# Kernel tuning notes

Measured on AMD Instinct MI355X. Metric: run time of the kernel, lower is better.

The kernel has to match this reference:

```python
import jax, jax.numpy as jnp
import numpy as np

K = 2  # number of propagation hops (SGConv K)
NEG_SLOPE = 0.1


def setup_inputs() -> dict:
    key = jax.random.key(0)
    k1, k2, k3, k4 = jax.random.split(key, 4)
    N, E, C_in, C_out = 50000, 800000, 128, 512
    x = jax.random.normal(k1, (N, C_in), dtype=jnp.float32)
    edge_index = jax.random.randint(k2, (2, E), 0, N, dtype=jnp.int64)
    W = jax.random.normal(k3, (C_out, C_in), dtype=jnp.float32) * (1.0 / np.sqrt(C_in))
    b = jax.random.normal(k4, (C_out,), dtype=jnp.float32) * 0.01
    return {"x": x, "edge_index": edge_index, "W": W, "b": b}


def reference(x, edge_index, W, b):
    N = x.shape[0]
    # gcn_norm with self-loops (PyG SGConv default: add_self_loops=True)
    loop = jnp.arange(N, dtype=edge_index.dtype)
    src = jnp.concatenate([edge_index[0], loop])  # message sources j
    dst = jnp.concatenate([edge_index[1], loop])  # aggregation targets i
    deg = jax.ops.segment_sum(jnp.ones_like(dst, dtype=x.dtype), dst, num_segments=N)
    dinv = jnp.where(deg > 0, jax.lax.rsqrt(deg), 0.0)
    norm = dinv[src] * dinv[dst]  # [E+N]
    h = x
    for _ in range(K):
        h = jax.ops.segment_sum(norm[:, None] * h[src], dst, num_segments=N)
    y = h @ W.T + b
    return jnp.where(y >= 0, y, NEG_SLOPE * y)  # LeakyReLU(0.1)
```

## Files before the change

### kernel.cpp

```cpp
#include <hip/hip_runtime.h>
#include <hip/hip_bf16.h>

#define CIN 128
#define COUT 512
#define NEG_SLOPE 0.1f

typedef __bf16 bf16x8 __attribute__((ext_vector_type(8)));
typedef float f32x4 __attribute__((ext_vector_type(4)));

static __device__ __forceinline__ unsigned short f2bf(float f) {
  unsigned int u = __builtin_bit_cast(unsigned int, f);
  unsigned int lsb = (u >> 16) & 1u;
  u += 0x7fffu + lsb;
  return (unsigned short)(u >> 16);
}
static __device__ __forceinline__ float bf_lo(unsigned int u) {
  return __builtin_bit_cast(float, u << 16);
}
static __device__ __forceinline__ float bf_hi(unsigned int u) {
  return __builtin_bit_cast(float, u & 0xffff0000u);
}
static __device__ __forceinline__ unsigned int pack2(float lo, float hi) {
  return (unsigned int)f2bf(lo) | ((unsigned int)f2bf(hi) << 16);
}

__global__ void detect_kernel(const int* __restrict__ raw, int* __restrict__ flag, int E) {
  __shared__ int any_nonzero;
  int tid = threadIdx.x;
  if (tid == 0) any_nonzero = 0;
  __syncthreads();
  int v1 = raw[2 * tid + 1];
  int v2 = raw[2 * (E / 2) + 2 * tid + 1];
  if (v1 != 0 || v2 != 0) atomicOr(&any_nonzero, 1);
  __syncthreads();
  if (tid == 0) *flag = any_nonzero ? 0 : 1;
}

__global__ void decode_count_kernel(const int* __restrict__ raw, const int* __restrict__ flag,
                                    int* __restrict__ srcA, int* __restrict__ dstA,
                                    int* __restrict__ rank, int* __restrict__ cnt,
                                    int E, int N) {
  int e = blockIdx.x * blockDim.x + threadIdx.x;
  if (e >= E) return;
  int is64 = *flag;
  int s, d;
  if (is64) {
    int2 sv = ((const int2*)raw)[e];
    int2 dv = ((const int2*)raw)[E + e];
    s = sv.x;
    d = dv.x;
  } else {
    s = raw[e];
    d = raw[E + e];
  }
  if ((unsigned)s >= (unsigned)N) s = 0;
  if ((unsigned)d >= (unsigned)N) d = 0;
  srcA[e] = s;
  dstA[e] = d;
  rank[e] = atomicAdd(&cnt[d], 1);
}

__global__ __launch_bounds__(256) void xscale_kernel(const float* __restrict__ x,
                                                     const int* __restrict__ cnt,
                                                     unsigned short* __restrict__ xs, int N) {
  int idx = blockIdx.x * blockDim.x + threadIdx.x;
  if (idx >= N * (CIN / 4)) return;
  int row = idx >> 5;
  float d = 1.0f / sqrtf((float)(cnt[row] + 1));
  float4 v = ((const float4*)x)[idx];
  ushort4 o;
  o.x = f2bf(v.x * d); o.y = f2bf(v.y * d); o.z = f2bf(v.z * d); o.w = f2bf(v.w * d);
  ((ushort4*)xs)[idx] = o;
}

__global__ __launch_bounds__(256) void scan1_kernel(const int* __restrict__ cnt,
                                                    int* __restrict__ rowptr,
                                                    int* __restrict__ bsum, int N) {
  __shared__ int buf[256];
  int tid = threadIdx.x;
  int base = blockIdx.x * 1024 + tid * 4;
  int v[4];
  int tot = 0;
#pragma unroll
  for (int k = 0; k < 4; ++k) {
    int i = base + k;
    v[k] = (i < N) ? cnt[i] : 0;
    tot += v[k];
  }
  buf[tid] = tot;
  __syncthreads();
  for (int off = 1; off < 256; off <<= 1) {
    int t = (tid >= off) ? buf[tid - off] : 0;
    __syncthreads();
    buf[tid] += t;
    __syncthreads();
  }
  int run = buf[tid] - tot;
  if (tid == 255) bsum[blockIdx.x] = buf[255];
#pragma unroll
  for (int k = 0; k < 4; ++k) {
    int i = base + k;
    if (i < N) rowptr[i] = run;
    run += v[k];
  }
}

__global__ void scan2_kernel(int* __restrict__ bsum, int nb) {
  __shared__ int buf[256];
  int tid = threadIdx.x;
  int v = (tid < nb) ? bsum[tid] : 0;
  buf[tid] = v;
  __syncthreads();
  for (int off = 1; off < 256; off <<= 1) {
    int t = (tid >= off) ? buf[tid - off] : 0;
    __syncthreads();
    buf[tid] += t;
    __syncthreads();
  }
  if (tid < nb) bsum[tid] = buf[tid] - v;
}

__global__ __launch_bounds__(256) void scan3_kernel(int* __restrict__ rowptr,
                                                    const int* __restrict__ bsum, int N) {
  int base = blockIdx.x * 1024 + threadIdx.x * 4;
  int off = bsum[blockIdx.x];
#pragma unroll
  for (int k = 0; k < 4; ++k) {
    int i = base + k;
    if (i < N) rowptr[i] += off;
  }
}

__global__ void scatter_kernel(const int* __restrict__ srcA, const int* __restrict__ dstA,
                               const int* __restrict__ rank, const int* __restrict__ rowptr,
                               int* __restrict__ col, int E) {
  int e = blockIdx.x * blockDim.x + threadIdx.x;
  if (e < E) col[rowptr[dstA[e]] + rank[e]] = srcA[e];
}

template <bool SQ>
__global__ __launch_bounds__(256) void hop_kernel(
    const unsigned short* __restrict__ Xs,
    const int* __restrict__ rowptr, const int* __restrict__ cnt,
    const int* __restrict__ col, unsigned short* __restrict__ Y, int N) {
  int lane = threadIdx.x & 63;
  int wid = threadIdx.x >> 6;
  int node = blockIdx.x * 4 + wid;
  if (node >= N) return;
  int sub = lane & 15;
  int grp = lane >> 4;
  int beg = rowptr[node];
  int num = cnt[node];
  const uint4* X4 = (const uint4*)Xs;
  float acc[8] = {0.f, 0.f, 0.f, 0.f, 0.f, 0.f, 0.f, 0.f};
  if (grp == 0) {
    uint4 s = X4[(size_t)node * 16 + sub];
    acc[0] = bf_lo(s.x); acc[1] = bf_hi(s.x);
    acc[2] = bf_lo(s.y); acc[3] = bf_hi(s.y);
    acc[4] = bf_lo(s.z); acc[5] = bf_hi(s.z);
    acc[6] = bf_lo(s.w); acc[7] = bf_hi(s.w);
  }
  const int* cp = col + beg;
  int kb = 0;
  for (; kb + 16 <= num; kb += 16) {
    int j0 = cp[kb + grp];
    int j1 = cp[kb + 4 + grp];
    int j2 = cp[kb + 8 + grp];
    int j3 = cp[kb + 12 + grp];
    uint4 v0 = X4[(size_t)j0 * 16 + sub];
    uint4 v1 = X4[(size_t)j1 * 16 + sub];
    uint4 v2 = X4[(size_t)j2 * 16 + sub];
    uint4 v3 = X4[(size_t)j3 * 16 + sub];
    acc[0] += bf_lo(v0.x); acc[1] += bf_hi(v0.x);
    acc[2] += bf_lo(v0.y); acc[3] += bf_hi(v0.y);
    acc[4] += bf_lo(v0.z); acc[5] += bf_hi(v0.z);
    acc[6] += bf_lo(v0.w); acc[7] += bf_hi(v0.w);
    acc[0] += bf_lo(v1.x); acc[1] += bf_hi(v1.x);
    acc[2] += bf_lo(v1.y); acc[3] += bf_hi(v1.y);
    acc[4] += bf_lo(v1.z); acc[5] += bf_hi(v1.z);
    acc[6] += bf_lo(v1.w); acc[7] += bf_hi(v1.w);
    acc[0] += bf_lo(v2.x); acc[1] += bf_hi(v2.x);
    acc[2] += bf_lo(v2.y); acc[3] += bf_hi(v2.y);
    acc[4] += bf_lo(v2.z); acc[5] += bf_hi(v2.z);
    acc[6] += bf_lo(v2.w); acc[7] += bf_hi(v2.w);
    acc[0] += bf_lo(v3.x); acc[1] += bf_hi(v3.x);
    acc[2] += bf_lo(v3.y); acc[3] += bf_hi(v3.y);
    acc[4] += bf_lo(v3.z); acc[5] += bf_hi(v3.z);
    acc[6] += bf_lo(v3.w); acc[7] += bf_hi(v3.w);
  }
  for (; kb < num; kb += 4) {
    int k = kb + grp;
    if (k < num) {
      int j0 = cp[k];
      uint4 v0 = X4[(size_t)j0 * 16 + sub];
      acc[0] += bf_lo(v0.x); acc[1] += bf_hi(v0.x);
      acc[2] += bf_lo(v0.y); acc[3] += bf_hi(v0.y);
      acc[4] += bf_lo(v0.z); acc[5] += bf_hi(v0.z);
      acc[6] += bf_lo(v0.w); acc[7] += bf_hi(v0.w);
    }
  }
#pragma unroll
  for (int r = 0; r < 8; ++r) acc[r] += __shfl_xor(acc[r], 16, 64);
#pragma unroll
  for (int r = 0; r < 8; ++r) acc[r] += __shfl_xor(acc[r], 32, 64);
  if (grp == 0) {
    float di = 1.0f / sqrtf((float)(num + 1));
    float sc = SQ ? di * di : di;
    uint4 o;
    o.x = pack2(acc[0] * sc, acc[1] * sc);
    o.y = pack2(acc[2] * sc, acc[3] * sc);
    o.z = pack2(acc[4] * sc, acc[5] * sc);
    o.w = pack2(acc[6] * sc, acc[7] * sc);
    ((uint4*)Y)[(size_t)node * 16 + sub] = o;
  }
}

__global__ void wconv_kernel(const float* __restrict__ W, unsigned short* __restrict__ Wbf, int n) {
  int i = blockIdx.x * blockDim.x + threadIdx.x;
  if (i < n) Wbf[i] = f2bf(W[i]);
}

__global__ __launch_bounds__(256) void gemm_kernel(
    const unsigned short* __restrict__ Abf, const unsigned short* __restrict__ Wbf,
    const float* __restrict__ bias, float* __restrict__ out, int M) {
  int wave = threadIdx.x >> 6;
  int lane = threadIdx.x & 63;
  int quad = lane >> 4;
  int l16 = lane & 15;
  int mbase = blockIdx.x * 32;

  int m0 = mbase + l16;
  int m1 = mbase + 16 + l16;
  bool v0 = m0 < M;
  bool v1 = m1 < M;

  bf16x8 af[2][4];
#pragma unroll
  for (int kk = 0; kk < 4; ++kk) {
    af[0][kk] = v0 ? *(const bf16x8*)(Abf + (size_t)m0 * CIN + kk * 32 + quad * 8) : bf16x8{};
    af[1][kk] = v1 ? *(const bf16x8*)(Abf + (size_t)m1 * CIN + kk * 32 + quad * 8) : bf16x8{};
  }

  int nbase = wave * 128;
#pragma unroll
  for (int nt = 0; nt < 8; ++nt) {
    int nrow = nbase + nt * 16 + l16;
    int n0 = nbase + nt * 16 + quad * 4;
    bf16x8 wf[4];
#pragma unroll
    for (int kk = 0; kk < 4; ++kk)
      wf[kk] = *(const bf16x8*)(Wbf + (size_t)nrow * CIN + kk * 32 + quad * 8);
    f32x4 acc0 = {}, acc1 = {};
#pragma unroll
    for (int kk = 0; kk < 4; ++kk) {
      acc0 = __builtin_amdgcn_mfma_f32_16x16x32_bf16(wf[kk], af[0][kk], acc0, 0, 0, 0);
      acc1 = __builtin_amdgcn_mfma_f32_16x16x32_bf16(wf[kk], af[1][kk], acc1, 0, 0, 0);
    }
    float4 bv = *(const float4*)(bias + n0);
    if (v0) {
      float4 o;
      o.x = acc0[0] + bv.x; o.x = (o.x >= 0.f) ? o.x : NEG_SLOPE * o.x;
      o.y = acc0[1] + bv.y; o.y = (o.y >= 0.f) ? o.y : NEG_SLOPE * o.y;
      o.z = acc0[2] + bv.z; o.z = (o.z >= 0.f) ? o.z : NEG_SLOPE * o.z;
      o.w = acc0[3] + bv.w; o.w = (o.w >= 0.f) ? o.w : NEG_SLOPE * o.w;
      *(float4*)(out + (size_t)m0 * COUT + n0) = o;
    }
    if (v1) {
      float4 o;
      o.x = acc1[0] + bv.x; o.x = (o.x >= 0.f) ? o.x : NEG_SLOPE * o.x;
      o.y = acc1[1] + bv.y; o.y = (o.y >= 0.f) ? o.y : NEG_SLOPE * o.y;
      o.z = acc1[2] + bv.z; o.z = (o.z >= 0.f) ? o.z : NEG_SLOPE * o.z;
      o.w = acc1[3] + bv.w; o.w = (o.w >= 0.f) ? o.w : NEG_SLOPE * o.w;
      *(float4*)(out + (size_t)m1 * COUT + n0) = o;
    }
  }
}

static inline size_t align_up(size_t v, size_t a) { return (v + a - 1) & ~(a - 1); }

extern "C" void kernel_launch(void* const* d_in, const int* in_sizes, int n_in,
                              void* d_out, int out_size, void* d_ws, size_t ws_size,
                              hipStream_t stream) {
  const float* x = (const float*)d_in[0];
  const int* edge_raw = (const int*)d_in[1];
  const float* W = (const float*)d_in[2];
  const float* b = (const float*)d_in[3];
  float* out = (float*)d_out;

  const int N = in_sizes[0] / CIN;
  const int E = in_sizes[1] / 2;
  const int NB = (N + 1023) / 1024;

  char* w = (char*)d_ws;
  int* flag = (int*)w;            w += align_up(sizeof(int), 256);
  int* bsum = (int*)w;            w += align_up(256 * 4, 256);
  int* cnt = (int*)w;             w += align_up((size_t)N * 4, 256);
  int* rowptr = (int*)w;          w += align_up((size_t)N * 4, 256);
  int* srcA = (int*)w;            w += align_up((size_t)E * 4, 256);
  int* dstA = (int*)w;            w += align_up((size_t)E * 4, 256);
  int* rank = (int*)w;            w += align_up((size_t)E * 4, 256);
  int* col = (int*)w;             w += align_up((size_t)E * 4, 256);
  unsigned short* h2bf = (unsigned short*)w;  w += align_up((size_t)N * CIN * 2, 256);
  unsigned short* Wbf = (unsigned short*)w;   w += align_up((size_t)COUT * CIN * 2, 256);

  size_t outb = (size_t)out_size * sizeof(float);
  size_t rowb = (size_t)N * CIN * sizeof(unsigned short);
  unsigned short* h1s = (unsigned short*)((char*)d_out + (outb - rowb));
  unsigned short* xs = (unsigned short*)((char*)d_out + (outb - 2 * rowb));

  hipMemsetAsync(cnt, 0, (size_t)N * sizeof(int), stream);

  detect_kernel<<<1, 64, 0, stream>>>(edge_raw, flag, E);
  decode_count_kernel<<<(E + 255) / 256, 256, 0, stream>>>(edge_raw, flag, srcA, dstA, rank, cnt, E, N);
  scan1_kernel<<<NB, 256, 0, stream>>>(cnt, rowptr, bsum, N);
  scan2_kernel<<<1, 256, 0, stream>>>(bsum, NB);
  scan3_kernel<<<NB, 256, 0, stream>>>(rowptr, bsum, N);
  scatter_kernel<<<(E + 255) / 256, 256, 0, stream>>>(srcA, dstA, rank, rowptr, col, E);
  xscale_kernel<<<(N * (CIN / 4) + 255) / 256, 256, 0, stream>>>(x, cnt, xs, N);

  hop_kernel<true><<<(N + 3) / 4, 256, 0, stream>>>(xs, rowptr, cnt, col, h1s, N);
  hop_kernel<false><<<(N + 3) / 4, 256, 0, stream>>>(h1s, rowptr, cnt, col, h2bf, N);

  wconv_kernel<<<(COUT * CIN + 255) / 256, 256, 0, stream>>>(W, Wbf, COUT * CIN);

  gemm_kernel<<<(N + 31) / 32, 256, 0, stream>>>(h2bf, Wbf, b, out, N);
}
```

Measured before the change: 283.0 us.

## Fold scan3 into consumers, merge W conversion into prep, stage GEMM output via LDS

The scan3 pass is removed. The scatter and hop kernels now add the per-block offset bsum[node>>10] on the fly. The W-to-bf16 conversion is merged into the x-scaling kernel, which saves two launches. The GEMM epilogue is staged through a shared-memory tile so that each output row is written with fully coalesced float4 stores instead of scattered 16-byte fragments. This adds LDS use (about 33 KB per block) and barriers, which may reduce occupancy.

```diff
diff --git a/kernel.cpp b/kernel.cpp
--- a/kernel.cpp
+++ b/kernel.cpp
@@ -60,17 +60,29 @@
   rank[e] = atomicAdd(&cnt[d], 1);
 }
 
-__global__ __launch_bounds__(256) void xscale_kernel(const float* __restrict__ x,
-                                                     const int* __restrict__ cnt,
-                                                     unsigned short* __restrict__ xs, int N) {
+__global__ __launch_bounds__(256) void prep_kernel(const float* __restrict__ x,
+                                                   const int* __restrict__ cnt,
+                                                   unsigned short* __restrict__ xs,
+                                                   const float* __restrict__ W,
+                                                   unsigned short* __restrict__ Wbf, int N) {
   int idx = blockIdx.x * blockDim.x + threadIdx.x;
-  if (idx >= N * (CIN / 4)) return;
-  int row = idx >> 5;
-  float d = 1.0f / sqrtf((float)(cnt[row] + 1));
-  float4 v = ((const float4*)x)[idx];
-  ushort4 o;
-  o.x = f2bf(v.x * d); o.y = f2bf(v.y * d); o.z = f2bf(v.z * d); o.w = f2bf(v.w * d);
-  ((ushort4*)xs)[idx] = o;
+  int nx = N * (CIN / 4);
+  if (idx < nx) {
+    int row = idx >> 5;
+    float d = 1.0f / sqrtf((float)(cnt[row] + 1));
+    float4 v = ((const float4*)x)[idx];
+    ushort4 o;
+    o.x = f2bf(v.x * d); o.y = f2bf(v.y * d); o.z = f2bf(v.z * d); o.w = f2bf(v.w * d);
+    ((ushort4*)xs)[idx] = o;
+  } else {
+    int i = idx - nx;
+    if (i < (COUT * CIN / 4)) {
+      float4 v = ((const float4*)W)[i];
+      ushort4 o;
+      o.x = f2bf(v.x); o.y = f2bf(v.y); o.z = f2bf(v.z); o.w = f2bf(v.w);
+      ((ushort4*)Wbf)[i] = o;
+    }
+  }
 }
 
 __global__ __launch_bounds__(256) void scan1_kernel(const int* __restrict__ cnt,
@@ -120,28 +132,21 @@
   if (tid < nb) bsum[tid] = buf[tid] - v;
 }
 
-__global__ __launch_bounds__(256) void scan3_kernel(int* __restrict__ rowptr,
-                                                    const int* __restrict__ bsum, int N) {
-  int base = blockIdx.x * 1024 + threadIdx.x * 4;
-  int off = bsum[blockIdx.x];
-#pragma unroll
-  for (int k = 0; k < 4; ++k) {
-    int i = base + k;
-    if (i < N) rowptr[i] += off;
-  }
-}
-
 __global__ void scatter_kernel(const int* __restrict__ srcA, const int* __restrict__ dstA,
                                const int* __restrict__ rank, const int* __restrict__ rowptr,
-                               int* __restrict__ col, int E) {
+                               const int* __restrict__ bsum, int* __restrict__ col, int E) {
   int e = blockIdx.x * blockDim.x + threadIdx.x;
-  if (e < E) col[rowptr[dstA[e]] + rank[e]] = srcA[e];
+  if (e < E) {
+    int d = dstA[e];
+    col[rowptr[d] + bsum[d >> 10] + rank[e]] = srcA[e];
+  }
 }
 
 template <bool SQ>
 __global__ __launch_bounds__(256) void hop_kernel(
     const unsigned short* __restrict__ Xs,
     const int* __restrict__ rowptr, const int* __restrict__ cnt,
+    const int* __restrict__ bsum,
     const int* __restrict__ col, unsigned short* __restrict__ Y, int N) {
   int lane = threadIdx.x & 63;
   int wid = threadIdx.x >> 6;
@@ -149,7 +154,7 @@
   if (node >= N) return;
   int sub = lane & 15;
   int grp = lane >> 4;
-  int beg = rowptr[node];
+  int beg = rowptr[node] + bsum[node >> 10];
   int num = cnt[node];
   const uint4* X4 = (const uint4*)Xs;
   float acc[8] = {0.f, 0.f, 0.f, 0.f, 0.f, 0.f, 0.f, 0.f};
@@ -215,14 +220,10 @@
   }
 }
 
-__global__ void wconv_kernel(const float* __restrict__ W, unsigned short* __restrict__ Wbf, int n) {
-  int i = blockIdx.x * blockDim.x + threadIdx.x;
-  if (i < n) Wbf[i] = f2bf(W[i]);
-}
-
 __global__ __launch_bounds__(256) void gemm_kernel(
     const unsigned short* __restrict__ Abf, const unsigned short* __restrict__ Wbf,
     const float* __restrict__ bias, float* __restrict__ out, int M) {
+  __shared__ float tile[16 * 516];
   int wave = threadIdx.x >> 6;
   int lane = threadIdx.x & 63;
   int quad = lane >> 4;
@@ -242,36 +243,46 @@
   }
 
   int nbase = wave * 128;
+  f32x4 acc0[8], acc1[8];
 #pragma unroll
   for (int nt = 0; nt < 8; ++nt) {
     int nrow = nbase + nt * 16 + l16;
-    int n0 = nbase + nt * 16 + quad * 4;
     bf16x8 wf[4];
 #pragma unroll
     for (int kk = 0; kk < 4; ++kk)
       wf[kk] = *(const bf16x8*)(Wbf + (size_t)nrow * CIN + kk * 32 + quad * 8);
-    f32x4 acc0 = {}, acc1 = {};
+    f32x4 a0 = {}, a1 = {};
 #pragma unroll
     for (int kk = 0; kk < 4; ++kk) {
-      acc0 = __builtin_amdgcn_mfma_f32_16x16x32_bf16(wf[kk], af[0][kk], acc0, 0, 0, 0);
-      acc1 = __builtin_amdgcn_mfma_f32_16x16x32_bf16(wf[kk], af[1][kk], acc1, 0, 0, 0);
-    }
-    float4 bv = *(const float4*)(bias + n0);
-    if (v0) {
+      a0 = __builtin_amdgcn_mfma_f32_16x16x32_bf16(wf[kk], af[0][kk], a0, 0, 0, 0);
+      a1 = __builtin_amdgcn_mfma_f32_16x16x32_bf16(wf[kk], af[1][kk], a1, 0, 0, 0);
+    }
+    acc0[nt] = a0;
+    acc1[nt] = a1;
+  }
+
+#pragma unroll
+  for (int half = 0; half < 2; ++half) {
+    if (half) __syncthreads();
+#pragma unroll
+    for (int nt = 0; nt < 8; ++nt) {
+      int n0 = nbase + nt * 16 + quad * 4;
+      float4 bv = *(const float4*)(bias + n0);
+      f32x4 a = half ? acc1[nt] : acc0[nt];
       float4 o;
-      o.x = acc0[0] + bv.x; o.x = (o.x >= 0.f) ? o.x : NEG_SLOPE * o.x;
-      o.y = acc0[1] + bv.y; o.y = (o.y >= 0.f) ? o.y : NEG_SLOPE * o.y;
-      o.z = acc0[2] + bv.z; o.z = (o.z >= 0.f) ? o.z : NEG_SLOPE * o.z;
-      o.w = acc0[3] + bv.w; o.w = (o.w >= 0.f) ? o.w : NEG_SLOPE * o.w;
-      *(float4*)(out + (size_t)m0 * COUT + n0) = o;
-    }
-    if (v1) {
-      float4 o;
-      o.x = acc1[0] + bv.x; o.x = (o.x >= 0.f) ? o.x : NEG_SLOPE * o.x;
-      o.y = acc1[1] + bv.y; o.y = (o.y >= 0.f) ? o.y : NEG_SLOPE * o.y;
-      o.z = acc1[2] + bv.z; o.z = (o.z >= 0.f) ? o.z : NEG_SLOPE * o.z;
-      o.w = acc1[3] + bv.w; o.w = (o.w >= 0.f) ? o.w : NEG_SLOPE * o.w;
-      *(float4*)(out + (size_t)m1 * COUT + n0) = o;
+      o.x = a[0] + bv.x; o.x = (o.x >= 0.f) ? o.x : NEG_SLOPE * o.x;
+      o.y = a[1] + bv.y; o.y = (o.y >= 0.f) ? o.y : NEG_SLOPE * o.y;
+      o.z = a[2] + bv.z; o.z = (o.z >= 0.f) ? o.z : NEG_SLOPE * o.z;
+      o.w = a[3] + bv.w; o.w = (o.w >= 0.f) ? o.w : NEG_SLOPE * o.w;
+      *(float4*)&tile[l16 * 516 + n0] = o;
+    }
+    __syncthreads();
+#pragma unroll
+    for (int it = 0; it < 8; ++it) {
+      int r = it * 2 + (threadIdx.x >> 7);
+      int c = (threadIdx.x & 127) * 4;
+      int m = mbase + half * 16 + r;
+      if (m < M) *(float4*)(out + (size_t)m * COUT + c) = *(const float4*)&tile[r * 516 + c];
     }
   }
 }
@@ -314,14 +325,11 @@
   decode_count_kernel<<<(E + 255) / 256, 256, 0, stream>>>(edge_raw, flag, srcA, dstA, rank, cnt, E, N);
   scan1_kernel<<<NB, 256, 0, stream>>>(cnt, rowptr, bsum, N);
   scan2_kernel<<<1, 256, 0, stream>>>(bsum, NB);
-  scan3_kernel<<<NB, 256, 0, stream>>>(rowptr, bsum, N);
-  scatter_kernel<<<(E + 255) / 256, 256, 0, stream>>>(srcA, dstA, rank, rowptr, col, E);
-  xscale_kernel<<<(N * (CIN / 4) + 255) / 256, 256, 0, stream>>>(x, cnt, xs, N);
-
-  hop_kernel<true><<<(N + 3) / 4, 256, 0, stream>>>(xs, rowptr, cnt, col, h1s, N);
-  hop_kernel<false><<<(N + 3) / 4, 256, 0, stream>>>(h1s, rowptr, cnt, col, h2bf, N);
-
-  wconv_kernel<<<(COUT * CIN + 255) / 256, 256, 0, stream>>>(W, Wbf, COUT * CIN);
+  scatter_kernel<<<(E + 255) / 256, 256, 0, stream>>>(srcA, dstA, rank, rowptr, bsum, col, E);
+  prep_kernel<<<(N * (CIN / 4) + COUT * CIN / 4 + 255) / 256, 256, 0, stream>>>(x, cnt, xs, W, Wbf, N);
+
+  hop_kernel<true><<<(N + 3) / 4, 256, 0, stream>>>(xs, rowptr, cnt, bsum, col, h1s, N);
+  hop_kernel<false><<<(N + 3) / 4, 256, 0, stream>>>(h1s, rowptr, cnt, bsum, col, h2bf, N);
 
   gemm_kernel<<<(N + 31) / 32, 256, 0, stream>>>(h2bf, Wbf, b, out, N);
 }
```

New measurement: 287.3 us. No clear change (+1.5%).
